# Optimization experiments

Measured on AMD Instinct MI355X. Metric: run time of the kernel, lower is better.

The kernel has to match this reference:

```python
import jax, jax.numpy as jnp
import numpy as np
from jax import lax

DIM = 256
QK = 256
HEADS = 8
NWIN = 7
TOPK = 4
KS = 5
SCALE = QK ** (-0.5)


def setup_inputs() -> dict:
    key = jax.random.key(0)
    ks = jax.random.split(key, 5)
    N, H, W = 8, 56, 56
    x = jax.random.normal(ks[0], (N, H, W, DIM), jnp.float32)
    W_qkv = jax.random.normal(ks[1], (DIM, QK + QK + DIM), jnp.float32) * 0.02
    b_qkv = jnp.zeros((QK + QK + DIM,), jnp.float32)
    lepe_w = jax.random.normal(ks[2], (DIM, 1, KS, KS), jnp.float32) * 0.05  # OIHW depthwise
    lepe_b = jnp.zeros((DIM,), jnp.float32)
    W_o = jax.random.normal(ks[3], (DIM, DIM), jnp.float32) * 0.02
    b_o = jnp.zeros((DIM,), jnp.float32)
    return {"x": x, "W_qkv": W_qkv, "b_qkv": b_qkv, "lepe_w": lepe_w,
            "lepe_b": lepe_b, "W_o": W_o, "b_o": b_o}


def reference(x, W_qkv, b_qkv, lepe_w, lepe_b, W_o, b_o):
    N, H, Wd, C = x.shape
    j = i = NWIN
    h, w = H // j, Wd // i
    p2, w2 = j * i, h * w
    hd, hdv = QK // HEADS, DIM // HEADS

    # window partition: n (j h) (i w) c -> n (j i) h w c
    xw = x.reshape(N, j, h, i, w, C).transpose(0, 1, 3, 2, 4, 5).reshape(N, p2, h, w, C)

    qkv = xw @ W_qkv + b_qkv                       # [N, p2, h, w, 2*QK+DIM... actually QK+(QK+DIM)]
    q = qkv[..., :QK]                              # [N, p2, h, w, QK]
    kv = qkv[..., QK:]                             # [N, p2, h, w, QK+DIM]

    q_pix = q.reshape(N, p2, w2, QK)
    kv_pix = kv.reshape(N, p2, w2, QK + DIM)       # identity kv_down

    q_win = q.mean(axis=(2, 3))                    # [N, p2, QK]
    k_win = kv[..., :QK].mean(axis=(2, 3))         # [N, p2, QK]

    # LePE: depthwise conv on v, in image layout
    v_img = kv[..., QK:].reshape(N, j, i, h, w, DIM).transpose(0, 5, 1, 3, 2, 4).reshape(N, DIM, H, Wd)
    pad = KS // 2
    lepe = lax.conv_general_dilated(v_img, lepe_w, (1, 1), [(pad, pad), (pad, pad)],
                                    feature_group_count=DIM)
    lepe = lepe + lepe_b[None, :, None, None]
    lepe = lepe.transpose(0, 2, 3, 1)              # [N, H, W, DIM]

    # coarse routing (detached in original when diff_routing=False)
    qd = lax.stop_gradient(q_win)
    kd = lax.stop_gradient(k_win)
    logit = jnp.einsum('npc,nqc->npq', qd * SCALE, kd)   # [N, p2, p2]
    _, r_idx = lax.top_k(logit, TOPK)              # [N, p2, TOPK]

    # gather top-k windows of kv (mul_weight='none')
    nidx = jnp.arange(N)[:, None, None]
    kv_sel = kv_pix[nidx, r_idx]                   # [N, p2, TOPK, w2, QK+DIM]
    k_sel = kv_sel[..., :QK].reshape(N, p2, TOPK * w2, HEADS, hd).transpose(0, 1, 3, 2, 4)
    v_sel = kv_sel[..., QK:].reshape(N, p2, TOPK * w2, HEADS, hdv).transpose(0, 1, 3, 2, 4)
    qh = q_pix.reshape(N, p2, w2, HEADS, hd).transpose(0, 1, 3, 2, 4)

    attn = jax.nn.softmax(jnp.einsum('npmwc,npmkc->npmwk', qh * SCALE, k_sel), axis=-1)
    out = jnp.einsum('npmwk,npmkc->npmwc', attn, v_sel)  # [N, p2, HEADS, w2, hdv]

    # back to image: (n p2) m (h w) c -> n (j h) (i w) (m c)
    out = out.transpose(0, 1, 3, 2, 4).reshape(N, j, i, h, w, DIM)
    out = out.transpose(0, 1, 3, 2, 4, 5).reshape(N, H, Wd, DIM)

    out = out + lepe
    out = out @ W_o + b_o
    return out
```

## Files before the change

### kernel.cpp

```cpp
#include <hip/hip_runtime.h>
#include <hip/hip_bf16.h>
#include <math.h>

#define NBATCH 8
#define HWDIM  56
#define NWIN   7
#define P2     49
#define HEADS  8
#define TOPK   4
#define SCALE  0.0625f
#define NPIX   (NBATCH*HWDIM*HWDIM)

typedef __attribute__((ext_vector_type(8))) short bf16x8;
typedef __attribute__((ext_vector_type(4))) float f32x4;

#define GLOBAL_AS __attribute__((address_space(1)))
#define LDS_AS    __attribute__((address_space(3)))

__device__ __forceinline__ void gload16(const unsigned short* g, unsigned short* l) {
  __builtin_amdgcn_global_load_lds((const GLOBAL_AS unsigned int*)g,
                                   (LDS_AS unsigned int*)l, 16, 0, 0);
}

__device__ __forceinline__ unsigned short f2bf(float f) {
  __hip_bfloat16 h = __float2bfloat16(f);
  return *reinterpret_cast<unsigned short*>(&h);
}
__device__ __forceinline__ float bf2f(unsigned short h) {
  return __uint_as_float(((unsigned)h) << 16);
}

__global__ __launch_bounds__(256) void convert_x(
    const float* __restrict__ xin, unsigned short* __restrict__ xb)
{
  const int i = (blockIdx.x * 256 + threadIdx.x) * 8;
  float4 a = *(const float4*)&xin[i];
  float4 b = *(const float4*)&xin[i + 4];
  ushort4 o0 = { f2bf(a.x), f2bf(a.y), f2bf(a.z), f2bf(a.w) };
  ushort4 o1 = { f2bf(b.x), f2bf(b.y), f2bf(b.z), f2bf(b.w) };
  *(ushort4*)&xb[i] = o0;
  *(ushort4*)&xb[i + 4] = o1;
}

__global__ __launch_bounds__(256) void prep_w(
    const float* __restrict__ W_qkv, const float* __restrict__ b_qkv,
    const float* __restrict__ W_o, const float* __restrict__ lepe_w,
    unsigned short* __restrict__ Wt_qkv, unsigned short* __restrict__ Wt_o,
    float* __restrict__ b_s, float* __restrict__ Wc)
{
  const int idx = blockIdx.x * 256 + threadIdx.x;
  if (idx < 768 * 256) {
    const int nn = idx >> 8, cc = idx & 255;
    float v = W_qkv[cc * 768 + nn];
    if (nn < 256) v *= SCALE;
    Wt_qkv[idx] = f2bf(v);
  } else if (idx < 768 * 256 + 256 * 256) {
    const int j = idx - 768 * 256;
    const int nn = j >> 8, cc = j & 255;
    Wt_o[j] = f2bf(W_o[cc * 256 + nn]);
  } else if (idx < 768 * 256 + 256 * 256 + 768) {
    const int j = idx - (768 * 256 + 256 * 256);
    b_s[j] = b_qkv[j] * (j < 256 ? SCALE : 1.f);
  } else if (idx < 768 * 256 + 256 * 256 + 768 + 25 * 256) {
    const int j = idx - (768 * 256 + 256 * 256 + 768);
    const int tap = j >> 8, cc = j & 255;
    Wc[j] = lepe_w[cc * 25 + tap];
  }
}

__global__ __launch_bounds__(256) void x_win_kernel(
    const float* __restrict__ x, float* __restrict__ xw)
{
  __shared__ float4 red[256];
  const int bidx = blockIdx.x;
  const int n = bidx / P2, p = bidx - n * P2;
  const int y0 = (p / NWIN) * 8, x0 = (p % NWIN) * 8;
  const int t = threadIdx.x;
  const int c4 = t & 63, pg = t >> 6;
  float4 s = {0.f, 0.f, 0.f, 0.f};
  #pragma unroll
  for (int k = 0; k < 16; ++k) {
    const int pix = pg * 16 + k;
    const int yy = y0 + (pix >> 3), xx = x0 + (pix & 7);
    float4 v = *(const float4*)&x[((size_t)((n * HWDIM + yy) * HWDIM + xx)) * 256 + c4 * 4];
    s.x += v.x; s.y += v.y; s.z += v.z; s.w += v.w;
  }
  red[t] = s;
  __syncthreads();
  if (pg == 0) {
    float4 a = red[c4], b = red[64 + c4], c = red[128 + c4], d = red[192 + c4];
    float4 o = { (a.x + b.x + c.x + d.x) * (1.f/64.f),
                 (a.y + b.y + c.y + d.y) * (1.f/64.f),
                 (a.z + b.z + c.z + d.z) * (1.f/64.f),
                 (a.w + b.w + c.w + d.w) * (1.f/64.f) };
    *(float4*)&xw[(size_t)bidx * 256 + c4 * 4] = o;
  }
}

__global__ __launch_bounds__(256) void win_gemm(
    const float* __restrict__ xw, const float* __restrict__ W_qkv,
    const float* __restrict__ b_qkv,
    float* __restrict__ q_win, float* __restrict__ k_win)
{
  __shared__ float xs[256];
  const int bidx = blockIdx.x;
  const int t = threadIdx.x;
  xs[t] = xw[(size_t)bidx * 256 + t];
  __syncthreads();
  float aq = 0.f, ak = 0.f;
  for (int cc = 0; cc < 256; ++cc) {
    const float xv = xs[cc];
    aq = fmaf(xv, W_qkv[cc * 768 + t], aq);
    ak = fmaf(xv, W_qkv[cc * 768 + 256 + t], ak);
  }
  q_win[(size_t)bidx * 256 + t] = aq + b_qkv[t];
  k_win[(size_t)bidx * 256 + t] = ak + b_qkv[256 + t];
}

__global__ __launch_bounds__(256) void routing_topk(
    const float* __restrict__ q_win, const float* __restrict__ k_win,
    int* __restrict__ r_idx)
{
  __shared__ float qs[256];
  __shared__ float logit[64];
  const int bidx = blockIdx.x;
  const int n = bidx / P2;
  const int t = threadIdx.x;
  qs[t] = q_win[(size_t)bidx * 256 + t];
  __syncthreads();
  const int qq = t >> 2, qt = t & 3;
  if (qq < P2) {
    const float* kb = k_win + ((size_t)(n * P2 + qq)) * 256 + qt * 64;
    float a = 0.f;
    #pragma unroll 8
    for (int i = 0; i < 64; ++i) a = fmaf(qs[qt * 64 + i], kb[i], a);
    a += __shfl_xor(a, 1);
    a += __shfl_xor(a, 2);
    if (qt == 0) logit[qq] = a;
  }
  __syncthreads();
  if (t == 0) {
    float bv0 = -3e38f, bv1 = -3e38f, bv2 = -3e38f, bv3 = -3e38f;
    int bi0 = 0, bi1 = 0, bi2 = 0, bi3 = 0;
    for (int q2 = 0; q2 < P2; ++q2) {
      const float v = logit[q2];
      if (v > bv0) { bv3=bv2; bi3=bi2; bv2=bv1; bi2=bi1; bv1=bv0; bi1=bi0; bv0=v; bi0=q2; }
      else if (v > bv1) { bv3=bv2; bi3=bi2; bv2=bv1; bi2=bi1; bv1=v; bi1=q2; }
      else if (v > bv2) { bv3=bv2; bi3=bi2; bv2=v; bi2=q2; }
      else if (v > bv3) { bv3=v; bi3=q2; }
    }
    int* rp = r_idx + (size_t)bidx * TOPK;
    rp[0] = bi0; rp[1] = bi1; rp[2] = bi2; rp[3] = bi3;
  }
}

template<int MODE>
__global__ __launch_bounds__(256) void gemm_mfma(
    const unsigned short* __restrict__ A,
    const unsigned short* __restrict__ Bt,
    const float* __restrict__ bias,
    unsigned short* __restrict__ C0, unsigned short* __restrict__ C1,
    unsigned short* __restrict__ C2, float* __restrict__ Cf)
{
  __shared__ char smem[32768];
  unsigned short* Asm = (unsigned short*)smem;
  unsigned short* Bsm = (unsigned short*)(smem + 16384);
  float* Cs = (float*)smem;

  const int t = threadIdx.x;
  const int w = t >> 6, l = t & 63;
  const int wr = w >> 1, wc = w & 1;
  const int lr = l & 15, lg = l >> 4;
  const int bm = blockIdx.x, bn = blockIdx.y;
  const int row0 = bm * 128, col0 = bn * 128;

  const f32x4 fzero = {0.f, 0.f, 0.f, 0.f};
  f32x4 acc[4][4];
  #pragma unroll
  for (int m = 0; m < 4; ++m)
    #pragma unroll
    for (int n = 0; n < 4; ++n) acc[m][n] = fzero;

  const int srow  = t >> 3;
  const int skoff = ((t & 7) ^ (srow & 7)) * 8;

  for (int step = 0; step < 4; ++step) {
    const int k0 = step * 64;
    #pragma unroll
    for (int i = 0; i < 4; ++i) {
      gload16(&A [(size_t)(row0 + i*32 + srow) * 256 + k0 + skoff], Asm + i*2048 + t*8);
      gload16(&Bt[(size_t)(col0 + i*32 + srow) * 256 + k0 + skoff], Bsm + i*2048 + t*8);
    }
    __syncthreads();
    #pragma unroll
    for (int kk = 0; kk < 2; ++kk) {
      bf16x8 af[4], bb[4];
      #pragma unroll
      for (int m = 0; m < 4; ++m)
        af[m] = *(const bf16x8*)&Asm[(wr*64 + m*16 + lr) * 64 + ((kk*4 + lg) ^ (lr & 7)) * 8];
      #pragma unroll
      for (int n = 0; n < 4; ++n)
        bb[n] = *(const bf16x8*)&Bsm[(wc*64 + n*16 + lr) * 64 + ((kk*4 + lg) ^ (lr & 7)) * 8];
      #pragma unroll
      for (int m = 0; m < 4; ++m)
        #pragma unroll
        for (int n = 0; n < 4; ++n)
          acc[m][n] = __builtin_amdgcn_mfma_f32_16x16x32_bf16(af[m], bb[n], acc[m][n], 0, 0, 0);
    }
    __syncthreads();
  }

  float bcol[4];
  #pragma unroll
  for (int n = 0; n < 4; ++n) bcol[n] = bias[col0 + wc*64 + n*16 + lr];

  #pragma unroll
  for (int hf = 0; hf < 2; ++hf) {
    if (hf) __syncthreads();
    if (wr == hf) {
      #pragma unroll
      for (int m = 0; m < 4; ++m)
        #pragma unroll
        for (int n = 0; n < 4; ++n)
          #pragma unroll
          for (int r = 0; r < 4; ++r) {
            const int lrow = m*16 + lg*4 + r;
            const int col  = wc*64 + n*16 + lr;
            const int csw  = col ^ ((lrow & 7) << 2);
            Cs[lrow * 128 + csw] = acc[m][n][r] + bcol[n];
          }
    }
    __syncthreads();
    #pragma unroll
    for (int it = 0; it < 8; ++it) {
      const int d = (it * 256 + t) * 4;
      const int lrow = d >> 7;
      const int colL = (d & 127) ^ ((lrow & 7) << 2);
      f32x4 v = *(const f32x4*)&Cs[d];
      const size_t grow = (size_t)(row0 + hf*64 + lrow);
      if (MODE == 0) {
        unsigned short* Cp = (bn < 2) ? C0 : (bn < 4) ? C1 : C2;
        const int lc = (bn & 1) * 128 + colL;
        ushort4 o = { f2bf(v[0]), f2bf(v[1]), f2bf(v[2]), f2bf(v[3]) };
        *(ushort4*)&Cp[grow * 256 + lc] = o;
      } else {
        float4 o = { v[0], v[1], v[2], v[3] };
        *(float4*)&Cf[grow * 256 + (size_t)(bn * 128) + colL] = o;
      }
    }
  }
}

#define PSTR 272

__global__ __launch_bounds__(256) void attn_mfma(
    const unsigned short* __restrict__ q_bf,
    const unsigned short* __restrict__ k_bf,
    const unsigned short* __restrict__ v_bf,
    const int* __restrict__ r_idx,
    unsigned short* __restrict__ o_bf)
{
  __shared__ char smem[52480];
  unsigned short* Ksm = (unsigned short*)smem;
  unsigned short* Qsm = (unsigned short*)(smem + 16384);
  unsigned short* Psm = (unsigned short*)smem;
  unsigned short* Vsm = (unsigned short*)(smem + 34816);
  float*          Osm = (float*)(smem + 34816);
  float*          Ls  = (float*)(smem + 52224);

  const int b = blockIdx.x;
  const int h = b & 7;
  const int np = b >> 3;
  const int n = np / P2, p = np - n * P2;
  const int t = threadIdx.x;
  const int w = t >> 6, l = t & 63;
  const int lr = l & 15, lg = l >> 4;

  const int4 rv = *(const int4*)&r_idx[np * 4];

  {
    const int pix = t >> 2, ch = t & 3;
    #pragma unroll
    for (int i = 0; i < 4; ++i) {
      const int wv = (&rv.x)[i];
      const int ky = (wv / NWIN) * 8 + (pix >> 3);
      const int kx = (wv % NWIN) * 8 + (pix & 7);
      const size_t goff = ((size_t)((n * HWDIM + ky) * HWDIM + kx)) * 256 + h * 32;
      gload16(&k_bf[goff + ch * 8], Ksm + i * 2048 + t * 8);
    }
    const int qy = (p / NWIN) * 8 + (pix >> 3);
    const int qx = (p % NWIN) * 8 + (pix & 7);
    gload16(&q_bf[((size_t)((n * HWDIM + qy) * HWDIM + qx)) * 256 + h * 32 + ch * 8],
            Qsm + t * 8);
  }
  {
    const int s = t >> 6, pix = t & 63;
    const int wv = (&rv.x)[s];
    const int ky = (wv / NWIN) * 8 + (pix >> 3);
    const int kx = (wv % NWIN) * 8 + (pix & 7);
    const size_t goff = ((size_t)((n * HWDIM + ky) * HWDIM + kx)) * 256 + h * 32;
    #pragma unroll
    for (int j = 0; j < 4; ++j) {
      bf16x8 vv = *(const bf16x8*)&v_bf[goff + j * 8];
      #pragma unroll
      for (int e = 0; e < 8; ++e)
        Vsm[(j * 8 + e) * PSTR + t] = (unsigned short)vv[e];
    }
  }
  __syncthreads();

  f32x4 sf[16];
  {
    const f32x4 fzero = {0.f, 0.f, 0.f, 0.f};
    bf16x8 aq = *(const bf16x8*)&Qsm[(w * 16 + lr) * 32 + lg * 8];
    #pragma unroll
    for (int f = 0; f < 16; ++f) {
      bf16x8 bk = *(const bf16x8*)&Ksm[(f * 16 + lr) * 32 + lg * 8];
      sf[f] = __builtin_amdgcn_mfma_f32_16x16x32_bf16(bk, aq, fzero, 0, 0, 0);
    }
  }

  {
    float mx = sf[0][0];
    #pragma unroll
    for (int f = 0; f < 16; ++f)
      #pragma unroll
      for (int r = 0; r < 4; ++r) mx = fmaxf(mx, sf[f][r]);
    mx = fmaxf(mx, __shfl_xor(mx, 16));
    mx = fmaxf(mx, __shfl_xor(mx, 32));
    float sum = 0.f;
    #pragma unroll
    for (int f = 0; f < 16; ++f)
      #pragma unroll
      for (int r = 0; r < 4; ++r) {
        float e = __expf(sf[f][r] - mx);
        sf[f][r] = e; sum += e;
      }
    sum += __shfl_xor(sum, 16);
    sum += __shfl_xor(sum, 32);
    if (lg == 0) Ls[w * 16 + lr] = 1.f / sum;
  }
  __syncthreads();

  #pragma unroll
  for (int f = 0; f < 16; ++f) {
    ushort4 pk = { f2bf(sf[f][0]), f2bf(sf[f][1]), f2bf(sf[f][2]), f2bf(sf[f][3]) };
    *(ushort4*)&Psm[(w * 16 + lr) * PSTR + f * 16 + lg * 4] = pk;
  }

  f32x4 oacc[2];
  oacc[0] = (f32x4){0.f, 0.f, 0.f, 0.f};
  oacc[1] = (f32x4){0.f, 0.f, 0.f, 0.f};
  #pragma unroll
  for (int ks = 0; ks < 8; ++ks) {
    bf16x8 ap = *(const bf16x8*)&Psm[(w * 16 + lr) * PSTR + ks * 32 + lg * 8];
    #pragma unroll
    for (int nn = 0; nn < 2; ++nn) {
      bf16x8 bv = *(const bf16x8*)&Vsm[(nn * 16 + lr) * PSTR + ks * 32 + lg * 8];
      oacc[nn] = __builtin_amdgcn_mfma_f32_16x16x32_bf16(ap, bv, oacc[nn], 0, 0, 0);
    }
  }

  float inv4[4];
  #pragma unroll
  for (int r = 0; r < 4; ++r) inv4[r] = Ls[w * 16 + lg * 4 + r];

  __syncthreads();
  #pragma unroll
  for (int nn = 0; nn < 2; ++nn)
    #pragma unroll
    for (int r = 0; r < 4; ++r)
      Osm[(w * 16 + lg * 4 + r) * 36 + nn * 16 + lr] = oacc[nn][r] * inv4[r];
  __syncthreads();
  {
    const int q = t >> 2, dq = (t & 3) * 8;
    const int qy = (p / NWIN) * 8 + (q >> 3);
    const int qx = (p % NWIN) * 8 + (q & 7);
    float vo[8];
    #pragma unroll
    for (int e = 0; e < 8; ++e) vo[e] = Osm[q * 36 + dq + e];
    ushort4 o0 = { f2bf(vo[0]), f2bf(vo[1]), f2bf(vo[2]), f2bf(vo[3]) };
    ushort4 o1 = { f2bf(vo[4]), f2bf(vo[5]), f2bf(vo[6]), f2bf(vo[7]) };
    unsigned short* op = &o_bf[((size_t)((n * HWDIM + qy) * HWDIM + qx)) * 256 + h * 32 + dq];
    *(ushort4*)op = o0;
    *(ushort4*)&op[4] = o1;
  }
}

__global__ __launch_bounds__(256) void lepe_add(
    const unsigned short* __restrict__ v_bf, const float* __restrict__ Wc,
    const float* __restrict__ bias, unsigned short* __restrict__ o_bf)
{
  const int gid = blockIdx.x * 256 + threadIdx.x;
  const int c8 = (gid & 31) * 8;
  const int pix = gid >> 5;
  const int n = pix / (HWDIM * HWDIM);
  const int rem = pix - n * (HWDIM * HWDIM);
  const int y = rem / HWDIM, x = rem - y * HWDIM;

  float acc[8];
  {
    float4 b0 = *(const float4*)&bias[c8];
    float4 b1 = *(const float4*)&bias[c8 + 4];
    acc[0]=b0.x; acc[1]=b0.y; acc[2]=b0.z; acc[3]=b0.w;
    acc[4]=b1.x; acc[5]=b1.y; acc[6]=b1.z; acc[7]=b1.w;
  }

  #pragma unroll
  for (int ky = 0; ky < 5; ++ky) {
    const int sy = y + ky - 2;
    if (sy < 0 || sy >= HWDIM) continue;
    #pragma unroll
    for (int kx = 0; kx < 5; ++kx) {
      const int sx = x + kx - 2;
      if (sx < 0 || sx >= HWDIM) continue;
      const bf16x8 vv = *(const bf16x8*)&v_bf[((size_t)((n * HWDIM + sy) * HWDIM + sx)) * 256 + c8];
      const float* wp = &Wc[(ky * 5 + kx) * 256 + c8];
      float4 w0 = *(const float4*)wp;
      float4 w1 = *(const float4*)(wp + 4);
      acc[0] = fmaf(w0.x, bf2f((unsigned short)vv[0]), acc[0]);
      acc[1] = fmaf(w0.y, bf2f((unsigned short)vv[1]), acc[1]);
      acc[2] = fmaf(w0.z, bf2f((unsigned short)vv[2]), acc[2]);
      acc[3] = fmaf(w0.w, bf2f((unsigned short)vv[3]), acc[3]);
      acc[4] = fmaf(w1.x, bf2f((unsigned short)vv[4]), acc[4]);
      acc[5] = fmaf(w1.y, bf2f((unsigned short)vv[5]), acc[5]);
      acc[6] = fmaf(w1.z, bf2f((unsigned short)vv[6]), acc[6]);
      acc[7] = fmaf(w1.w, bf2f((unsigned short)vv[7]), acc[7]);
    }
  }

  unsigned short* op = &o_bf[(size_t)pix * 256 + c8];
  const bf16x8 ov = *(const bf16x8*)op;
  ushort4 o0 = { f2bf(bf2f((unsigned short)ov[0]) + acc[0]),
                 f2bf(bf2f((unsigned short)ov[1]) + acc[1]),
                 f2bf(bf2f((unsigned short)ov[2]) + acc[2]),
                 f2bf(bf2f((unsigned short)ov[3]) + acc[3]) };
  ushort4 o1 = { f2bf(bf2f((unsigned short)ov[4]) + acc[4]),
                 f2bf(bf2f((unsigned short)ov[5]) + acc[5]),
                 f2bf(bf2f((unsigned short)ov[6]) + acc[6]),
                 f2bf(bf2f((unsigned short)ov[7]) + acc[7]) };
  *(ushort4*)op = o0;
  *(ushort4*)(op + 4) = o1;
}

extern "C" void kernel_launch(void* const* d_in, const int* in_sizes, int n_in,
                              void* d_out, int out_size, void* d_ws, size_t ws_size,
                              hipStream_t stream)
{
  const float* x      = (const float*)d_in[0];
  const float* W_qkv  = (const float*)d_in[1];
  const float* b_qkv  = (const float*)d_in[2];
  const float* lepe_w = (const float*)d_in[3];
  const float* lepe_b = (const float*)d_in[4];
  const float* W_o    = (const float*)d_in[5];
  const float* b_o    = (const float*)d_in[6];
  float* out = (float*)d_out;

  char* ws = (char*)d_ws;
  const size_t IMG = (size_t)NPIX * 256;
  unsigned short* x_bf    = (unsigned short*)(ws);
  unsigned short* q_bf    = (unsigned short*)(ws + 2*IMG);
  unsigned short* k_bf    = (unsigned short*)(ws + 4*IMG);
  unsigned short* v_bf    = (unsigned short*)(ws + 6*IMG);
  unsigned short* attn_bf = (unsigned short*)(ws + 8*IMG);
  unsigned short* Wt_qkv  = (unsigned short*)(ws + 10*IMG);
  unsigned short* Wt_o    = (unsigned short*)(ws + 10*IMG + 393216);
  float*          b_s     = (float*)         (ws + 10*IMG + 393216 + 131072);
  float*          x_win   = (float*)         (ws + 10*IMG + 393216 + 131072 + 4096);
  float*          q_win   = x_win + (size_t)NBATCH * P2 * 256;
  float*          k_win   = q_win + (size_t)NBATCH * P2 * 256;
  int*            ridx    = (int*)(k_win + (size_t)NBATCH * P2 * 256);
  float*          Wc      = (float*)(ridx + (size_t)NBATCH * P2 * TOPK);

  convert_x<<<3136, 256, 0, stream>>>(x, x_bf);
  prep_w<<<1052, 256, 0, stream>>>(W_qkv, b_qkv, W_o, lepe_w, Wt_qkv, Wt_o, b_s, Wc);
  x_win_kernel<<<NBATCH * P2, 256, 0, stream>>>(x, x_win);
  win_gemm<<<NBATCH * P2, 256, 0, stream>>>(x_win, W_qkv, b_qkv, q_win, k_win);
  routing_topk<<<NBATCH * P2, 256, 0, stream>>>(q_win, k_win, ridx);
  gemm_mfma<0><<<dim3(196, 6), 256, 0, stream>>>(x_bf, Wt_qkv, b_s,
                                                 q_bf, k_bf, v_bf, nullptr);
  attn_mfma<<<NBATCH * P2 * HEADS, 256, 0, stream>>>(q_bf, k_bf, v_bf, ridx, attn_bf);
  lepe_add<<<3136, 256, 0, stream>>>(v_bf, Wc, lepe_b, attn_bf);
  gemm_mfma<1><<<dim3(196, 2), 256, 0, stream>>>(attn_bf, Wt_o, b_o,
                                                 nullptr, nullptr, nullptr, out);
}
```

Before: 219.2 us.

## Fuse x conversion with window mean and widen GEMM tiles to 128x256

Merges the fp32-to-bf16 conversion of x with the per-window mean kernel, so x is read from memory once instead of twice and one launch is dropped. The MFMA GEMM moves from 128x128 tiles with 256 threads to 128x256 tiles with 512 threads (8 waves). Each block now covers a full 256-column output slab, which halves the grid and reuses each A tile across twice as many columns. The trade-off is fewer blocks, which lowers parallelism for the output projection (196 blocks), plus a larger shared-memory footprint.

```diff
diff --git a/kernel.cpp b/kernel.cpp
--- a/kernel.cpp
+++ b/kernel.cpp
@@ -30,16 +30,37 @@
   return __uint_as_float(((unsigned)h) << 16);
 }
 
-__global__ __launch_bounds__(256) void convert_x(
-    const float* __restrict__ xin, unsigned short* __restrict__ xb)
-{
-  const int i = (blockIdx.x * 256 + threadIdx.x) * 8;
-  float4 a = *(const float4*)&xin[i];
-  float4 b = *(const float4*)&xin[i + 4];
-  ushort4 o0 = { f2bf(a.x), f2bf(a.y), f2bf(a.z), f2bf(a.w) };
-  ushort4 o1 = { f2bf(b.x), f2bf(b.y), f2bf(b.z), f2bf(b.w) };
-  *(ushort4*)&xb[i] = o0;
-  *(ushort4*)&xb[i + 4] = o1;
+__global__ __launch_bounds__(256) void conv_xwin(
+    const float* __restrict__ x, unsigned short* __restrict__ xb,
+    float* __restrict__ xw)
+{
+  __shared__ float4 red[256];
+  const int bidx = blockIdx.x;
+  const int n = bidx / P2, p = bidx - n * P2;
+  const int y0 = (p / NWIN) * 8, x0 = (p % NWIN) * 8;
+  const int t = threadIdx.x;
+  const int c4 = t & 63, pg = t >> 6;
+  float4 s = {0.f, 0.f, 0.f, 0.f};
+  #pragma unroll
+  for (int k = 0; k < 16; ++k) {
+    const int pix = pg * 16 + k;
+    const int yy = y0 + (pix >> 3), xx = x0 + (pix & 7);
+    const size_t off = ((size_t)((n * HWDIM + yy) * HWDIM + xx)) * 256 + c4 * 4;
+    float4 v = *(const float4*)&x[off];
+    ushort4 o = { f2bf(v.x), f2bf(v.y), f2bf(v.z), f2bf(v.w) };
+    *(ushort4*)&xb[off] = o;
+    s.x += v.x; s.y += v.y; s.z += v.z; s.w += v.w;
+  }
+  red[t] = s;
+  __syncthreads();
+  if (pg == 0) {
+    float4 a = red[c4], b = red[64 + c4], c = red[128 + c4], d = red[192 + c4];
+    float4 o = { (a.x + b.x + c.x + d.x) * (1.f/64.f),
+                 (a.y + b.y + c.y + d.y) * (1.f/64.f),
+                 (a.z + b.z + c.z + d.z) * (1.f/64.f),
+                 (a.w + b.w + c.w + d.w) * (1.f/64.f) };
+    *(float4*)&xw[(size_t)bidx * 256 + c4 * 4] = o;
+  }
 }
 
 __global__ __launch_bounds__(256) void prep_w(
@@ -68,35 +89,6 @@
   }
 }
 
-__global__ __launch_bounds__(256) void x_win_kernel(
-    const float* __restrict__ x, float* __restrict__ xw)
-{
-  __shared__ float4 red[256];
-  const int bidx = blockIdx.x;
-  const int n = bidx / P2, p = bidx - n * P2;
-  const int y0 = (p / NWIN) * 8, x0 = (p % NWIN) * 8;
-  const int t = threadIdx.x;
-  const int c4 = t & 63, pg = t >> 6;
-  float4 s = {0.f, 0.f, 0.f, 0.f};
-  #pragma unroll
-  for (int k = 0; k < 16; ++k) {
-    const int pix = pg * 16 + k;
-    const int yy = y0 + (pix >> 3), xx = x0 + (pix & 7);
-    float4 v = *(const float4*)&x[((size_t)((n * HWDIM + yy) * HWDIM + xx)) * 256 + c4 * 4];
-    s.x += v.x; s.y += v.y; s.z += v.z; s.w += v.w;
-  }
-  red[t] = s;
-  __syncthreads();
-  if (pg == 0) {
-    float4 a = red[c4], b = red[64 + c4], c = red[128 + c4], d = red[192 + c4];
-    float4 o = { (a.x + b.x + c.x + d.x) * (1.f/64.f),
-                 (a.y + b.y + c.y + d.y) * (1.f/64.f),
-                 (a.z + b.z + c.z + d.z) * (1.f/64.f),
-                 (a.w + b.w + c.w + d.w) * (1.f/64.f) };
-    *(float4*)&xw[(size_t)bidx * 256 + c4 * 4] = o;
-  }
-}
-
 __global__ __launch_bounds__(256) void win_gemm(
     const float* __restrict__ xw, const float* __restrict__ W_qkv,
     const float* __restrict__ b_qkv,
@@ -155,24 +147,24 @@
 }
 
 template<int MODE>
-__global__ __launch_bounds__(256) void gemm_mfma(
+__global__ __launch_bounds__(512) void gemm_mfma(
     const unsigned short* __restrict__ A,
     const unsigned short* __restrict__ Bt,
     const float* __restrict__ bias,
     unsigned short* __restrict__ C0, unsigned short* __restrict__ C1,
     unsigned short* __restrict__ C2, float* __restrict__ Cf)
 {
-  __shared__ char smem[32768];
+  __shared__ char smem[49152];
   unsigned short* Asm = (unsigned short*)smem;
   unsigned short* Bsm = (unsigned short*)(smem + 16384);
   float* Cs = (float*)smem;
 
   const int t = threadIdx.x;
   const int w = t >> 6, l = t & 63;
-  const int wr = w >> 1, wc = w & 1;
+  const int wr = w >> 2, wc = w & 3;
   const int lr = l & 15, lg = l >> 4;
   const int bm = blockIdx.x, bn = blockIdx.y;
-  const int row0 = bm * 128, col0 = bn * 128;
+  const int row0 = bm * 128, col0 = bn * 256;
 
   const f32x4 fzero = {0.f, 0.f, 0.f, 0.f};
   f32x4 acc[4][4];
@@ -187,10 +179,13 @@
   for (int step = 0; step < 4; ++step) {
     const int k0 = step * 64;
     #pragma unroll
-    for (int i = 0; i < 4; ++i) {
-      gload16(&A [(size_t)(row0 + i*32 + srow) * 256 + k0 + skoff], Asm + i*2048 + t*8);
-      gload16(&Bt[(size_t)(col0 + i*32 + srow) * 256 + k0 + skoff], Bsm + i*2048 + t*8);
-    }
+    for (int i = 0; i < 2; ++i)
+      gload16(&A [(size_t)(row0 + i*64 + srow) * 256 + k0 + skoff],
+              Asm + i*4096 + t*8);
+    #pragma unroll
+    for (int i = 0; i < 4; ++i)
+      gload16(&Bt[(size_t)(col0 + i*64 + srow) * 256 + k0 + skoff],
+              Bsm + i*4096 + t*8);
     __syncthreads();
     #pragma unroll
     for (int kk = 0; kk < 2; ++kk) {
@@ -215,37 +210,37 @@
   for (int n = 0; n < 4; ++n) bcol[n] = bias[col0 + wc*64 + n*16 + lr];
 
   #pragma unroll
-  for (int hf = 0; hf < 2; ++hf) {
+  for (int hf = 0; hf < 4; ++hf) {
     if (hf) __syncthreads();
-    if (wr == hf) {
-      #pragma unroll
-      for (int m = 0; m < 4; ++m)
+    if (wr == (hf >> 1)) {
+      const int mbase = (hf & 1) * 2;
+      #pragma unroll
+      for (int mm = 0; mm < 2; ++mm)
         #pragma unroll
         for (int n = 0; n < 4; ++n)
           #pragma unroll
           for (int r = 0; r < 4; ++r) {
-            const int lrow = m*16 + lg*4 + r;
+            const int lrow = mm*16 + lg*4 + r;
             const int col  = wc*64 + n*16 + lr;
             const int csw  = col ^ ((lrow & 7) << 2);
-            Cs[lrow * 128 + csw] = acc[m][n][r] + bcol[n];
+            Cs[lrow * 256 + csw] = acc[mbase + mm][n][r] + bcol[n];
           }
     }
     __syncthreads();
     #pragma unroll
-    for (int it = 0; it < 8; ++it) {
-      const int d = (it * 256 + t) * 4;
-      const int lrow = d >> 7;
-      const int colL = (d & 127) ^ ((lrow & 7) << 2);
+    for (int it = 0; it < 4; ++it) {
+      const int d = (it * 512 + t) * 4;
+      const int lrow = d >> 8;
+      const int colL = (d & 255) ^ ((lrow & 7) << 2);
       f32x4 v = *(const f32x4*)&Cs[d];
-      const size_t grow = (size_t)(row0 + hf*64 + lrow);
+      const size_t grow = (size_t)(row0 + hf*32 + lrow);
       if (MODE == 0) {
-        unsigned short* Cp = (bn < 2) ? C0 : (bn < 4) ? C1 : C2;
-        const int lc = (bn & 1) * 128 + colL;
+        unsigned short* Cp = (bn == 0) ? C0 : (bn == 1) ? C1 : C2;
         ushort4 o = { f2bf(v[0]), f2bf(v[1]), f2bf(v[2]), f2bf(v[3]) };
-        *(ushort4*)&Cp[grow * 256 + lc] = o;
+        *(ushort4*)&Cp[grow * 256 + colL] = o;
       } else {
         float4 o = { v[0], v[1], v[2], v[3] };
-        *(float4*)&Cf[grow * 256 + (size_t)(bn * 128) + colL] = o;
+        *(float4*)&Cf[grow * 256 + colL] = o;
       }
     }
   }
@@ -472,15 +467,14 @@
   int*            ridx    = (int*)(k_win + (size_t)NBATCH * P2 * 256);
   float*          Wc      = (float*)(ridx + (size_t)NBATCH * P2 * TOPK);
 
-  convert_x<<<3136, 256, 0, stream>>>(x, x_bf);
+  conv_xwin<<<NBATCH * P2, 256, 0, stream>>>(x, x_bf, x_win);
   prep_w<<<1052, 256, 0, stream>>>(W_qkv, b_qkv, W_o, lepe_w, Wt_qkv, Wt_o, b_s, Wc);
-  x_win_kernel<<<NBATCH * P2, 256, 0, stream>>>(x, x_win);
   win_gemm<<<NBATCH * P2, 256, 0, stream>>>(x_win, W_qkv, b_qkv, q_win, k_win);
   routing_topk<<<NBATCH * P2, 256, 0, stream>>>(q_win, k_win, ridx);
-  gemm_mfma<0><<<dim3(196, 6), 256, 0, stream>>>(x_bf, Wt_qkv, b_s,
+  gemm_mfma<0><<<dim3(196, 3), 512, 0, stream>>>(x_bf, Wt_qkv, b_s,
                                                  q_bf, k_bf, v_bf, nullptr);
   attn_mfma<<<NBATCH * P2 * HEADS, 256, 0, stream>>>(q_bf, k_bf, v_bf, ridx, attn_bf);
   lepe_add<<<3136, 256, 0, stream>>>(v_bf, Wc, lepe_b, attn_bf);
-  gemm_mfma<1><<<dim3(196, 2), 256, 0, stream>>>(attn_bf, Wt_o, b_o,
+  gemm_mfma<1><<<dim3(196, 1), 512, 0, stream>>>(attn_bf, Wt_o, b_o,
                                                  nullptr, nullptr, nullptr, out);
 }
```

Result: no change. 217.4 us (-0.8%).
